# Performance work log

Measured on AMD Instinct MI355X. Metric: run time of the kernel, lower is better.

The kernel has to match this reference:

```python
import jax, jax.numpy as jnp
import numpy as np

WINDOW_SIZES = (1, 2, 3)
ALPHA = 0.2          # LeakyReLU negative slope
NEG = -9e15          # mask fill value from the torch code


def _xavier(key, shape, gain=np.sqrt(2.0)):
    fan_in, fan_out = shape[0], shape[1]
    std = gain * np.sqrt(2.0 / (fan_in + fan_out))
    return jax.random.normal(key, shape, jnp.float32) * std


def setup_inputs() -> dict:
    key = jax.random.key(0)
    k1, k2, k3, k4, k5 = jax.random.split(key, 5)
    T, B, D, F = 512, 64, 256, 256  # turns, batch, input_dim, output_dim (must match)
    return {
        "local_semantic_vectors": jax.random.normal(k1, (T, B, D), jnp.float32),
        "input_turns": jax.random.randint(k2, (B,), 0, T),  # turns[bt] <= T-1
        "W": _xavier(k3, (D, F)),
        "a1": _xavier(k4, (F, 1)),
        "a2": _xavier(k5, (F, 1)),
    }


def _window_mean(x, w):
    # x: [B, T, D] -> sliding-window mean over axis 1 (window w), zero-padded at end.
    B, T, D = x.shape
    xp = jnp.pad(x, ((0, 0), (0, w - 1), (0, 0)))
    acc = xp[:, :T]
    for j in range(1, w):  # w <= 3, tiny unrolled loop
        acc = acc + xp[:, j:j + T]
    return acc / w


def reference(local_semantic_vectors, input_turns, W, a1, a2):
    # local_semantic_vectors: [T, B, D] -> [B, T, D]
    x = jnp.swapaxes(local_semantic_vectors, 0, 1)
    B, T, D = x.shape
    t_idx = jnp.arange(T)

    num = jnp.zeros((B, W.shape[1]), jnp.float32)
    vws = jnp.zeros((B,), jnp.float32)  # number of window sizes with cnt > 0

    for w in WINDOW_SIZES:
        # number of valid windows per sample: t runs while w+t-1 <= turns
        cnt = jnp.maximum(input_turns - w + 2, 0)                  # [B]
        valid = t_idx[None, :] < cnt[:, None]                      # [B, T]

        # pooled window vectors, zero beyond cnt (max_turn padded to T;
        # padded rows are fully masked and dropped, so the result matches)
        pooled = jnp.where(valid[:, :, None], _window_mean(x, w), 0.0)  # [B, T, D]

        # GAT-style masked self-attention
        h = pooled @ W                                             # [B, T, F]
        f1 = h @ a1                                                # [B, T, 1]
        f2 = h @ a2                                                # [B, T, 1]
        e = jax.nn.leaky_relu(f1 + jnp.swapaxes(f2, 1, 2), ALPHA)  # [B, T, T]
        mask = valid[:, :, None] & valid[:, None, :]
        attn = jax.nn.softmax(jnp.where(mask, e, NEG), axis=-1)
        h_prime = attn @ h                                         # [B, T, F]

        # mean over the first cnt rows
        denom = jnp.maximum(cnt, 1).astype(jnp.float32)
        inter = (h_prime * valid[:, :, None]).sum(axis=1) / denom[:, None]  # [B, F]

        has = (cnt > 0).astype(jnp.float32)
        num = num + inter * has[:, None]
        vws = vws + has

    # cnt is non-increasing in w, so windows with cnt>0 are exactly the first vws;
    # vws >= 1 always (w=1 gives cnt = turns + 2 >= 2).
    return num / vws[:, None]
```

## Files before the change

kernel.cpp:

```cpp
#include <hip/hip_runtime.h>
#include <math.h>

#define T_DIM 512
#define B_DIM 64
#define D_DIM 256
#define F_DIM 256
#define ALPHA 0.2f
#define L2E 1.44269504089f
#define NEGL -1.0e38f

#define U_OFF 0
#define V_OFF 256
#define P_OFF 512
#define Q_OFF (P_OFF + B_DIM * T_DIM)
#define FC_OFF (Q_OFF + B_DIM * T_DIM)

__device__ __forceinline__ float dot4(float4 a, float4 b) {
    return a.x * b.x + a.y * b.y + a.z * b.z + a.w * b.w;
}

__device__ __forceinline__ float dpp_sum(float x) {
    union { float f; int i; } a, t;
    a.f = x;
    t.i = __builtin_amdgcn_update_dpp(0, a.i, 0x111, 0xf, 0xf, true); a.f += t.f;
    t.i = __builtin_amdgcn_update_dpp(0, a.i, 0x112, 0xf, 0xf, true); a.f += t.f;
    t.i = __builtin_amdgcn_update_dpp(0, a.i, 0x114, 0xf, 0xf, true); a.f += t.f;
    t.i = __builtin_amdgcn_update_dpp(0, a.i, 0x118, 0xf, 0xf, true); a.f += t.f;
    t.i = __builtin_amdgcn_update_dpp(0, a.i, 0x142, 0xf, 0xf, true); a.f += t.f;
    t.i = __builtin_amdgcn_update_dpp(0, a.i, 0x143, 0xf, 0xf, true); a.f += t.f;
    return a.f;
}

__global__ __launch_bounds__(256) void g_uv(const float* __restrict__ W,
                                            const float* __restrict__ a1,
                                            const float* __restrict__ a2,
                                            float* __restrict__ ws,
                                            float* __restrict__ out) {
    int tid = threadIdx.x;
    out[blockIdx.x * 256 + tid] = 0.f;
    int wave = tid >> 6, lane = tid & 63;
    int d = blockIdx.x * 4 + wave;
    float4 wv = ((const float4*)(W + (size_t)d * F_DIM))[lane];
    float4 a1v = ((const float4*)a1)[lane];
    float4 a2v = ((const float4*)a2)[lane];
    float p = dpp_sum(dot4(wv, a1v));
    float q = dpp_sum(dot4(wv, a2v));
    if (lane == 63) {
        ws[U_OFF + d] = p;
        ws[V_OFF + d] = q;
    }
}

__global__ __launch_bounds__(512) void g_pq(const float* __restrict__ x,
                                            const int* __restrict__ turns,
                                            float* __restrict__ ws) {
    __shared__ float su[D_DIM], sv[D_DIM];
    int tid = threadIdx.x;
    if (tid < 64) ((float4*)su)[tid] = ((const float4*)(ws + U_OFF))[tid];
    else if (tid < 128) ((float4*)sv)[tid - 64] = ((const float4*)(ws + V_OFF))[tid - 64];
    __syncthreads();
    int lane = tid & 63;
    int gw = blockIdx.x * 8 + (tid >> 6);
    int b = gw & 63;
    int tbase = gw >> 6;
    int tn = turns[b];
    float4 uv = ((const float4*)su)[lane];
    float4 vv = ((const float4*)sv)[lane];
    float4 xv[8];
#pragma unroll
    for (int k = 0; k < 8; ++k) {
        int t = min(tbase + k * 64, tn);
        xv[k] = ((const float4*)x)[((size_t)t * B_DIM + b) * (D_DIM / 4) + lane];
    }
#pragma unroll
    for (int k = 0; k < 8; ++k) {
        int t = tbase + k * 64;
        if (t <= tn) {
            float pp = dpp_sum(dot4(xv[k], uv));
            float qq = dpp_sum(dot4(xv[k], vv));
            if (lane == 63) {
                ws[P_OFF + b * T_DIM + t] = pp;
                ws[Q_OFF + b * T_DIM + t] = qq;
            }
        }
    }
}

__global__ __launch_bounds__(1024) void g_row(const int* __restrict__ turns,
                                              float* __restrict__ ws) {
    int bi = blockIdx.x, tid = threadIdx.x;
    int b = bi / 12, rem = bi % 12;
    int w = (rem >> 2) + 1, ic = rem & 3;
    int tn = turns[b];
    int cnt = tn - w + 2;
    if (cnt > T_DIM) cnt = T_DIM;
    float2* FC = (float2*)(ws + FC_OFF) + ((w - 1) * B_DIM + b) * T_DIM;
    if (cnt <= 0) return;
    __shared__ float sp[T_DIM], sq[T_DIM], f2L[T_DIM];
    __shared__ float part[8][128];
    __shared__ float redm[8];
    if (tid < 128) ((float4*)sp)[tid] = ((const float4*)(ws + P_OFF + b * T_DIM))[tid];
    else if (tid < 256) ((float4*)sq)[tid - 128] = ((const float4*)(ws + Q_OFF + b * T_DIM))[tid - 128];
    __syncthreads();
    float scale = L2E / (float)w;
    int wave = tid >> 6, lane = tid & 63;
    if (tid < 512) {
        int j = tid;
        float v = NEGL;
        if (j < cnt) {
            float a = sq[j];
            if (w > 1) a += sq[j + 1];
            if (w > 2) a += sq[j + 2];
            v = a * scale;
        }
        f2L[j] = v;
        float m = v;
        for (int off = 32; off > 0; off >>= 1) m = fmaxf(m, __shfl_down(m, off));
        if (lane == 0) redm[wave] = m;
    }
    __syncthreads();
    float M = redm[0];
#pragma unroll
    for (int k = 1; k < 8; ++k) M = fmaxf(M, redm[k]);

    int il = tid & 127, oct = tid >> 7;
    int i = ic * 128 + il;
    float r = 0.f;
    if (i < cnt) {
        float a = sp[i];
        if (w > 1) a += sp[i + 1];
        if (w > 2) a += sp[i + 2];
        float f1 = a * scale;
        float s0 = f1 + M;
        float mrow = fmaxf(s0, ALPHA * s0);
        const float4* fv = (const float4*)(f2L + oct * 64);
#pragma unroll 4
        for (int k = 0; k < 16; ++k) {
            float4 f = fv[k];
            float sa = f1 + f.x, sb = f1 + f.y, sc = f1 + f.z, sd = f1 + f.w;
            sa = fmaxf(sa, ALPHA * sa); sb = fmaxf(sb, ALPHA * sb);
            sc = fmaxf(sc, ALPHA * sc); sd = fmaxf(sd, ALPHA * sd);
            r += __builtin_amdgcn_exp2f(sa - mrow) + __builtin_amdgcn_exp2f(sb - mrow)
               + __builtin_amdgcn_exp2f(sc - mrow) + __builtin_amdgcn_exp2f(sd - mrow);
        }
    }
    part[oct][il] = r;
    __syncthreads();
    if (tid < 128) {
        int i2 = ic * 128 + tid;
        float2 pr = make_float2(0.f, 3.0e38f);
        if (i2 < cnt) {
            float rt = part[0][tid];
#pragma unroll
            for (int k = 1; k < 8; ++k) rt += part[k][tid];
            float a = sp[i2];
            if (w > 1) a += sp[i2 + 1];
            if (w > 2) a += sp[i2 + 2];
            float f1 = a * scale;
            float s0 = f1 + M;
            float mrow = fmaxf(s0, ALPHA * s0);
            pr = make_float2(f1, mrow + __builtin_amdgcn_logf(rt));
        }
        FC[i2] = pr;
    }
}

__global__ __launch_bounds__(512) void g_colzout(const float* __restrict__ x,
                                                 const int* __restrict__ turns,
                                                 const float* __restrict__ W,
                                                 const float* __restrict__ ws,
                                                 float* __restrict__ out) {
    int b = blockIdx.x >> 2, chunk = blockIdx.x & 3;
    int tn = turns[b];
    int t0 = chunk * 128;
    if (t0 > tn) return;
    int tid = threadIdx.x;
    __shared__ float sq[T_DIM];
    __shared__ float4 fcs4[3][T_DIM / 2];
    __shared__ float Gs[3][132];
    __shared__ float partq[128][4];
    __shared__ float part2[2][128];
    __shared__ float Cs[128];
    __shared__ float4 zp[512];
    __shared__ float Zs[D_DIM];
    __shared__ float ored[512];

    if (tid < 128) ((float4*)sq)[tid] = ((const float4*)(ws + Q_OFF + b * T_DIM))[tid];
    for (int k = tid; k < 3 * 256; k += 512) {
        int wi = k >> 8, kk = k & 255;
        fcs4[wi][kk] = ((const float4*)(ws + FC_OFF))[(wi * B_DIM + b) * 256 + kk];
    }
    __syncthreads();

    for (int w = 1; w <= 3; ++w) {
        int cw = tn - w + 2;
        if (cw > T_DIM) cw = T_DIM;
        bool act = cw > 0;
        float scale = L2E / (float)w;
        if (act) {
            {
                int jj = tid >> 2, iq = tid & 3;
                int j = t0 + jj;
                float acc = 0.f;
                if (j < cw) {
                    float a = sq[j];
                    if (w > 1) a += sq[j + 1];
                    if (w > 2) a += sq[j + 2];
                    float f2j = a * scale;
                    const float4* fv = fcs4[w - 1] + iq * 64;
                    for (int k = 0; k < 64; ++k) {
                        float4 f = fv[k];
                        float sa = f.x + f2j, sb = f.z + f2j;
                        sa = fmaxf(sa, ALPHA * sa); sb = fmaxf(sb, ALPHA * sb);
                        acc += __builtin_amdgcn_exp2f(sa - f.y)
                             + __builtin_amdgcn_exp2f(sb - f.w);
                    }
                }
                partq[jj][iq] = acc;
            }
            if (tid < 256) {
                int e = tid >> 7, q2 = tid & 127;
                int j2 = t0 - 2 + e;
                float acc = 0.f;
                if (j2 >= 0 && j2 < cw) {
                    float a = sq[j2];
                    if (w > 1) a += sq[j2 + 1];
                    if (w > 2) a += sq[j2 + 2];
                    float f2j = a * scale;
                    const float4* fv = fcs4[w - 1] + q2 * 2;
#pragma unroll
                    for (int k = 0; k < 2; ++k) {
                        float4 f = fv[k];
                        float sa = f.x + f2j, sb = f.z + f2j;
                        sa = fmaxf(sa, ALPHA * sa); sb = fmaxf(sb, ALPHA * sb);
                        acc += __builtin_amdgcn_exp2f(sa - f.y)
                             + __builtin_amdgcn_exp2f(sb - f.w);
                    }
                }
                part2[e][q2] = acc;
            }
        }
        __syncthreads();
        if (act) {
            float invc = 1.0f / (float)cw;
            if (tid < 128) {
                int j = t0 + tid;
                float s = partq[tid][0] + partq[tid][1] + partq[tid][2] + partq[tid][3];
                Gs[w - 1][2 + tid] = (j < cw) ? s * invc : 0.f;
            } else if (tid < 130) {
                int e = tid - 128;
                int j2 = t0 - 2 + e;
                float s = 0.f;
                for (int k = 0; k < 128; ++k) s += part2[e][k];
                Gs[w - 1][e] = (j2 >= 0 && j2 < cw) ? s * invc : 0.f;
            }
        } else if (tid < 132) {
            Gs[w - 1][tid] = 0.f;
        }
        __syncthreads();
    }

    if (tid < 128) {
        float g1 = Gs[0][2 + tid];
        float g2 = Gs[1][2 + tid] + Gs[1][1 + tid];
        float g3 = Gs[2][2 + tid] + Gs[2][1 + tid] + Gs[2][tid];
        float vws = 1.f + (tn >= 1 ? 1.f : 0.f) + (tn >= 2 ? 1.f : 0.f);
        Cs[tid] = (g1 + 0.5f * g2 + (1.0f / 3.0f) * g3) / vws;
    }
    __syncthreads();

    int wave = tid >> 6, lane = tid & 63;
    float4 z = make_float4(0.f, 0.f, 0.f, 0.f);
    {
        size_t base = ((size_t)(t0 + wave * 16) * B_DIM + b) * (D_DIM / 4) + lane;
#pragma unroll 8
        for (int tt = 0; tt < 16; ++tt) {
            float c = Cs[wave * 16 + tt];
            float4 xv = ((const float4*)x)[base + (size_t)tt * (B_DIM * D_DIM / 4)];
            z.x += c * xv.x; z.y += c * xv.y; z.z += c * xv.z; z.w += c * xv.w;
        }
    }
    zp[tid] = z;
    __syncthreads();
    if (tid < 64) {
        float4 a = zp[tid];
#pragma unroll
        for (int k = 1; k < 8; ++k) {
            float4 bb = zp[k * 64 + tid];
            a.x += bb.x; a.y += bb.y; a.z += bb.z; a.w += bb.w;
        }
        ((float4*)Zs)[tid] = a;
    }
    __syncthreads();
    int f = tid & 255, dh = tid >> 8;
    float acc = 0.f;
#pragma unroll 8
    for (int dd = dh * 128; dd < dh * 128 + 128; ++dd)
        acc += Zs[dd] * W[(size_t)dd * F_DIM + f];
    ored[tid] = acc;
    __syncthreads();
    if (tid < 256)
        atomicAdd(&out[b * F_DIM + tid], ored[tid] + ored[tid + 256]);
}

extern "C" void kernel_launch(void* const* d_in, const int* in_sizes, int n_in,
                              void* d_out, int out_size, void* d_ws, size_t ws_size,
                              hipStream_t stream) {
    const float* x = (const float*)d_in[0];
    const int* turns = (const int*)d_in[1];
    const float* W = (const float*)d_in[2];
    const float* a1 = (const float*)d_in[3];
    const float* a2 = (const float*)d_in[4];
    float* out = (float*)d_out;
    float* ws = (float*)d_ws;

    g_uv<<<B_DIM, 256, 0, stream>>>(W, a1, a2, ws, out);
    g_pq<<<512, 512, 0, stream>>>(x, turns, ws);
    g_row<<<B_DIM * 12, 1024, 0, stream>>>(turns, ws);
    g_colzout<<<B_DIM * 4, 512, 0, stream>>>(x, turns, W, ws, out);
}
```

Measured before the change: 47.00 us.

## Fuse uv, pq and row-softmax kernels into one per-batch front kernel

Merges three kernels (W·a projection, per-turn p/q dot products, row log-sum-exp) into a single kernel with one 1024-thread block per batch element. Intermediates p, q, u and v stay in shared memory rather than round-tripping through global workspace, and two launches are removed. In exchange, every block recomputes W·a1/W·a2 redundantly and parallelism drops from hundreds of blocks to 64, each doing serial work over all three window sizes.

Result: slower. 74.52 us (+58.5%).

```diff
diff --git a/kernel.cpp b/kernel.cpp
--- a/kernel.cpp
+++ b/kernel.cpp
@@ -9,10 +9,7 @@
 #define L2E 1.44269504089f
 #define NEGL -1.0e38f
 
-#define U_OFF 0
-#define V_OFF 256
-#define P_OFF 512
-#define Q_OFF (P_OFF + B_DIM * T_DIM)
+#define Q_OFF 0
 #define FC_OFF (Q_OFF + B_DIM * T_DIM)
 
 __device__ __forceinline__ float dot4(float4 a, float4 b) {
@@ -31,137 +28,138 @@
     return a.f;
 }
 
-__global__ __launch_bounds__(256) void g_uv(const float* __restrict__ W,
-                                            const float* __restrict__ a1,
-                                            const float* __restrict__ a2,
-                                            float* __restrict__ ws,
-                                            float* __restrict__ out) {
-    int tid = threadIdx.x;
-    out[blockIdx.x * 256 + tid] = 0.f;
+__global__ __launch_bounds__(1024) void g_front(const float* __restrict__ x,
+                                                const int* __restrict__ turns,
+                                                const float* __restrict__ W,
+                                                const float* __restrict__ a1,
+                                                const float* __restrict__ a2,
+                                                float* __restrict__ ws,
+                                                float* __restrict__ out) {
+    int b = blockIdx.x, tid = threadIdx.x;
     int wave = tid >> 6, lane = tid & 63;
-    int d = blockIdx.x * 4 + wave;
-    float4 wv = ((const float4*)(W + (size_t)d * F_DIM))[lane];
-    float4 a1v = ((const float4*)a1)[lane];
-    float4 a2v = ((const float4*)a2)[lane];
-    float p = dpp_sum(dot4(wv, a1v));
-    float q = dpp_sum(dot4(wv, a2v));
-    if (lane == 63) {
-        ws[U_OFF + d] = p;
-        ws[V_OFF + d] = q;
-    }
-}
-
-__global__ __launch_bounds__(512) void g_pq(const float* __restrict__ x,
-                                            const int* __restrict__ turns,
-                                            float* __restrict__ ws) {
-    __shared__ float su[D_DIM], sv[D_DIM];
-    int tid = threadIdx.x;
-    if (tid < 64) ((float4*)su)[tid] = ((const float4*)(ws + U_OFF))[tid];
-    else if (tid < 128) ((float4*)sv)[tid - 64] = ((const float4*)(ws + V_OFF))[tid - 64];
-    __syncthreads();
-    int lane = tid & 63;
-    int gw = blockIdx.x * 8 + (tid >> 6);
-    int b = gw & 63;
-    int tbase = gw >> 6;
+    __shared__ float a1s[F_DIM], a2s[F_DIM], su[D_DIM], sv[D_DIM];
+    __shared__ float sp[T_DIM], sq[T_DIM], f2L[T_DIM];
+    __shared__ float part[2][T_DIM];
+    __shared__ float redm[8];
+
+    if (tid < 256) out[b * F_DIM + tid] = 0.f;
+    if (tid < 64) ((float4*)a1s)[tid] = ((const float4*)a1)[tid];
+    else if (tid < 128) ((float4*)a2s)[tid - 64] = ((const float4*)a2)[tid - 64];
+    __syncthreads();
+
+    {
+        float4 A = ((const float4*)a1s)[lane];
+        float4 Bv = ((const float4*)a2s)[lane];
+        float4 wv[8];
+#pragma unroll
+        for (int c = 0; c < 2; ++c) {
+#pragma unroll
+            for (int k = 0; k < 8; ++k) {
+                int d = wave + 16 * (c * 8 + k);
+                wv[k] = ((const float4*)(W + (size_t)d * F_DIM))[lane];
+            }
+#pragma unroll
+            for (int k = 0; k < 8; ++k) {
+                int d = wave + 16 * (c * 8 + k);
+                float p = dpp_sum(dot4(wv[k], A));
+                float q = dpp_sum(dot4(wv[k], Bv));
+                if (lane == 63) { su[d] = p; sv[d] = q; }
+            }
+        }
+    }
+    __syncthreads();
+
     int tn = turns[b];
-    float4 uv = ((const float4*)su)[lane];
-    float4 vv = ((const float4*)sv)[lane];
-    float4 xv[8];
-#pragma unroll
-    for (int k = 0; k < 8; ++k) {
-        int t = min(tbase + k * 64, tn);
-        xv[k] = ((const float4*)x)[((size_t)t * B_DIM + b) * (D_DIM / 4) + lane];
-    }
-#pragma unroll
-    for (int k = 0; k < 8; ++k) {
-        int t = tbase + k * 64;
-        if (t <= tn) {
-            float pp = dpp_sum(dot4(xv[k], uv));
-            float qq = dpp_sum(dot4(xv[k], vv));
-            if (lane == 63) {
-                ws[P_OFF + b * T_DIM + t] = pp;
-                ws[Q_OFF + b * T_DIM + t] = qq;
-            }
-        }
-    }
-}
-
-__global__ __launch_bounds__(1024) void g_row(const int* __restrict__ turns,
-                                              float* __restrict__ ws) {
-    int bi = blockIdx.x, tid = threadIdx.x;
-    int b = bi / 12, rem = bi % 12;
-    int w = (rem >> 2) + 1, ic = rem & 3;
-    int tn = turns[b];
-    int cnt = tn - w + 2;
-    if (cnt > T_DIM) cnt = T_DIM;
-    float2* FC = (float2*)(ws + FC_OFF) + ((w - 1) * B_DIM + b) * T_DIM;
-    if (cnt <= 0) return;
-    __shared__ float sp[T_DIM], sq[T_DIM], f2L[T_DIM];
-    __shared__ float part[8][128];
-    __shared__ float redm[8];
-    if (tid < 128) ((float4*)sp)[tid] = ((const float4*)(ws + P_OFF + b * T_DIM))[tid];
-    else if (tid < 256) ((float4*)sq)[tid - 128] = ((const float4*)(ws + Q_OFF + b * T_DIM))[tid - 128];
-    __syncthreads();
-    float scale = L2E / (float)w;
-    int wave = tid >> 6, lane = tid & 63;
-    if (tid < 512) {
-        int j = tid;
-        float v = NEGL;
-        if (j < cnt) {
-            float a = sq[j];
-            if (w > 1) a += sq[j + 1];
-            if (w > 2) a += sq[j + 2];
-            v = a * scale;
-        }
-        f2L[j] = v;
-        float m = v;
-        for (int off = 32; off > 0; off >>= 1) m = fmaxf(m, __shfl_down(m, off));
-        if (lane == 0) redm[wave] = m;
-    }
-    __syncthreads();
-    float M = redm[0];
-#pragma unroll
-    for (int k = 1; k < 8; ++k) M = fmaxf(M, redm[k]);
-
-    int il = tid & 127, oct = tid >> 7;
-    int i = ic * 128 + il;
-    float r = 0.f;
-    if (i < cnt) {
-        float a = sp[i];
-        if (w > 1) a += sp[i + 1];
-        if (w > 2) a += sp[i + 2];
-        float f1 = a * scale;
-        float s0 = f1 + M;
-        float mrow = fmaxf(s0, ALPHA * s0);
-        const float4* fv = (const float4*)(f2L + oct * 64);
+    {
+        float4 uu = ((const float4*)su)[lane];
+        float4 vv = ((const float4*)sv)[lane];
+        float4 xv[8];
+#pragma unroll
+        for (int c = 0; c < 4; ++c) {
+#pragma unroll
+            for (int k = 0; k < 8; ++k) {
+                int t = min(wave + 16 * (c * 8 + k), tn);
+                xv[k] = ((const float4*)x)[((size_t)t * B_DIM + b) * (D_DIM / 4) + lane];
+            }
+#pragma unroll
+            for (int k = 0; k < 8; ++k) {
+                int t = wave + 16 * (c * 8 + k);
+                if (t <= tn) {
+                    float pp = dpp_sum(dot4(xv[k], uu));
+                    float qq = dpp_sum(dot4(xv[k], vv));
+                    if (lane == 63) {
+                        sp[t] = pp; sq[t] = qq;
+                        ws[Q_OFF + b * T_DIM + t] = qq;
+                    }
+                }
+            }
+        }
+    }
+    __syncthreads();
+
+    for (int w = 1; w <= 3; ++w) {
+        int cnt = tn - w + 2;
+        if (cnt > T_DIM) cnt = T_DIM;
+        if (cnt <= 0) continue;
+        float scale = L2E / (float)w;
+        if (tid < 512) {
+            int j = tid;
+            float v = NEGL;
+            if (j < cnt) {
+                float a = sq[j];
+                if (w > 1) a += sq[j + 1];
+                if (w > 2) a += sq[j + 2];
+                v = a * scale;
+            }
+            f2L[j] = v;
+            float m = v;
+            for (int off = 32; off > 0; off >>= 1) m = fmaxf(m, __shfl_down(m, off));
+            if (lane == 0) redm[wave] = m;
+        }
+        __syncthreads();
+        float M = redm[0];
+#pragma unroll
+        for (int k = 1; k < 8; ++k) M = fmaxf(M, redm[k]);
+
+        {
+            int i = tid & 511, jh = tid >> 9;
+            float r = 0.f;
+            if (i < cnt) {
+                float a = sp[i];
+                if (w > 1) a += sp[i + 1];
+                if (w > 2) a += sp[i + 2];
+                float f1 = a * scale;
+                float s0 = f1 + M;
+                float mrow = fmaxf(s0, ALPHA * s0);
+                const float4* fv = (const float4*)(f2L + jh * 256);
 #pragma unroll 4
-        for (int k = 0; k < 16; ++k) {
-            float4 f = fv[k];
-            float sa = f1 + f.x, sb = f1 + f.y, sc = f1 + f.z, sd = f1 + f.w;
-            sa = fmaxf(sa, ALPHA * sa); sb = fmaxf(sb, ALPHA * sb);
-            sc = fmaxf(sc, ALPHA * sc); sd = fmaxf(sd, ALPHA * sd);
-            r += __builtin_amdgcn_exp2f(sa - mrow) + __builtin_amdgcn_exp2f(sb - mrow)
-               + __builtin_amdgcn_exp2f(sc - mrow) + __builtin_amdgcn_exp2f(sd - mrow);
-        }
-    }
-    part[oct][il] = r;
-    __syncthreads();
-    if (tid < 128) {
-        int i2 = ic * 128 + tid;
-        float2 pr = make_float2(0.f, 3.0e38f);
-        if (i2 < cnt) {
-            float rt = part[0][tid];
-#pragma unroll
-            for (int k = 1; k < 8; ++k) rt += part[k][tid];
-            float a = sp[i2];
-            if (w > 1) a += sp[i2 + 1];
-            if (w > 2) a += sp[i2 + 2];
-            float f1 = a * scale;
-            float s0 = f1 + M;
-            float mrow = fmaxf(s0, ALPHA * s0);
-            pr = make_float2(f1, mrow + __builtin_amdgcn_logf(rt));
-        }
-        FC[i2] = pr;
+                for (int k = 0; k < 64; ++k) {
+                    float4 f = fv[k];
+                    float sa = f1 + f.x, sb = f1 + f.y, sc = f1 + f.z, sd = f1 + f.w;
+                    sa = fmaxf(sa, ALPHA * sa); sb = fmaxf(sb, ALPHA * sb);
+                    sc = fmaxf(sc, ALPHA * sc); sd = fmaxf(sd, ALPHA * sd);
+                    r += __builtin_amdgcn_exp2f(sa - mrow) + __builtin_amdgcn_exp2f(sb - mrow)
+                       + __builtin_amdgcn_exp2f(sc - mrow) + __builtin_amdgcn_exp2f(sd - mrow);
+                }
+            }
+            part[jh][i] = r;
+        }
+        __syncthreads();
+        if (tid < 512) {
+            int i = tid;
+            float2 pr = make_float2(0.f, 3.0e38f);
+            if (i < cnt) {
+                float a = sp[i];
+                if (w > 1) a += sp[i + 1];
+                if (w > 2) a += sp[i + 2];
+                float f1 = a * scale;
+                float s0 = f1 + M;
+                float mrow = fmaxf(s0, ALPHA * s0);
+                pr = make_float2(f1, mrow + __builtin_amdgcn_logf(part[0][i] + part[1][i]));
+            }
+            ((float2*)(ws + FC_OFF))[((w - 1) * B_DIM + b) * T_DIM + i] = pr;
+        }
+        __syncthreads();
     }
 }
 
@@ -314,8 +312,6 @@
     float* out = (float*)d_out;
     float* ws = (float*)d_ws;
 
-    g_uv<<<B_DIM, 256, 0, stream>>>(W, a1, a2, ws, out);
-    g_pq<<<512, 512, 0, stream>>>(x, turns, ws);
-    g_row<<<B_DIM * 12, 1024, 0, stream>>>(turns, ws);
+    g_front<<<B_DIM, 1024, 0, stream>>>(x, turns, W, a1, a2, ws, out);
     g_colzout<<<B_DIM * 4, 512, 0, stream>>>(x, turns, W, ws, out);
 }
```

## Fuse p/q projection into row-softmax kernel, looping window sizes per block

Applied to the files above, without the earlier changes.

Merges the g_pq and g_row kernels into one g_rowpq kernel with 256 blocks, one per (batch, 128-row chunk). Each block recomputes q over all turns of its batch and p over its own row range (plus a halo) directly into shared memory, then loops over the three window sizes. This drops a kernel launch and the global round-trip of p. The cost is redundant reads of x and q dot products, since each batch's full q is recomputed by four blocks, and there are fewer blocks running serial work per window.

After: 56.40 us. +20.0%, slower.

```diff
diff --git a/kernel.cpp b/kernel.cpp
--- a/kernel.cpp
+++ b/kernel.cpp
@@ -11,8 +11,7 @@
 
 #define U_OFF 0
 #define V_OFF 256
-#define P_OFF 512
-#define Q_OFF (P_OFF + B_DIM * T_DIM)
+#define Q_OFF 512
 #define FC_OFF (Q_OFF + B_DIM * T_DIM)
 
 __device__ __forceinline__ float dot4(float4 a, float4 b) {
@@ -51,117 +50,129 @@
     }
 }
 
-__global__ __launch_bounds__(512) void g_pq(const float* __restrict__ x,
-                                            const int* __restrict__ turns,
-                                            float* __restrict__ ws) {
+__global__ __launch_bounds__(1024) void g_rowpq(const float* __restrict__ x,
+                                                const int* __restrict__ turns,
+                                                float* __restrict__ ws) {
+    int b = blockIdx.x >> 2, ic = blockIdx.x & 3;
+    int tid = threadIdx.x, wave = tid >> 6, lane = tid & 63;
+    int i0 = ic * 128;
     __shared__ float su[D_DIM], sv[D_DIM];
-    int tid = threadIdx.x;
-    if (tid < 64) ((float4*)su)[tid] = ((const float4*)(ws + U_OFF))[tid];
-    else if (tid < 128) ((float4*)sv)[tid - 64] = ((const float4*)(ws + V_OFF))[tid - 64];
-    __syncthreads();
-    int lane = tid & 63;
-    int gw = blockIdx.x * 8 + (tid >> 6);
-    int b = gw & 63;
-    int tbase = gw >> 6;
-    int tn = turns[b];
-    float4 uv = ((const float4*)su)[lane];
-    float4 vv = ((const float4*)sv)[lane];
-    float4 xv[8];
-#pragma unroll
-    for (int k = 0; k < 8; ++k) {
-        int t = min(tbase + k * 64, tn);
-        xv[k] = ((const float4*)x)[((size_t)t * B_DIM + b) * (D_DIM / 4) + lane];
-    }
-#pragma unroll
-    for (int k = 0; k < 8; ++k) {
-        int t = tbase + k * 64;
-        if (t <= tn) {
-            float pp = dpp_sum(dot4(xv[k], uv));
-            float qq = dpp_sum(dot4(xv[k], vv));
-            if (lane == 63) {
-                ws[P_OFF + b * T_DIM + t] = pp;
-                ws[Q_OFF + b * T_DIM + t] = qq;
-            }
-        }
-    }
-}
-
-__global__ __launch_bounds__(1024) void g_row(const int* __restrict__ turns,
-                                              float* __restrict__ ws) {
-    int bi = blockIdx.x, tid = threadIdx.x;
-    int b = bi / 12, rem = bi % 12;
-    int w = (rem >> 2) + 1, ic = rem & 3;
-    int tn = turns[b];
-    int cnt = tn - w + 2;
-    if (cnt > T_DIM) cnt = T_DIM;
-    float2* FC = (float2*)(ws + FC_OFF) + ((w - 1) * B_DIM + b) * T_DIM;
-    if (cnt <= 0) return;
     __shared__ float sp[T_DIM], sq[T_DIM], f2L[T_DIM];
     __shared__ float part[8][128];
     __shared__ float redm[8];
-    if (tid < 128) ((float4*)sp)[tid] = ((const float4*)(ws + P_OFF + b * T_DIM))[tid];
-    else if (tid < 256) ((float4*)sq)[tid - 128] = ((const float4*)(ws + Q_OFF + b * T_DIM))[tid - 128];
-    __syncthreads();
-    float scale = L2E / (float)w;
-    int wave = tid >> 6, lane = tid & 63;
-    if (tid < 512) {
-        int j = tid;
-        float v = NEGL;
-        if (j < cnt) {
-            float a = sq[j];
-            if (w > 1) a += sq[j + 1];
-            if (w > 2) a += sq[j + 2];
-            v = a * scale;
-        }
-        f2L[j] = v;
-        float m = v;
-        for (int off = 32; off > 0; off >>= 1) m = fmaxf(m, __shfl_down(m, off));
-        if (lane == 0) redm[wave] = m;
-    }
-    __syncthreads();
-    float M = redm[0];
-#pragma unroll
-    for (int k = 1; k < 8; ++k) M = fmaxf(M, redm[k]);
-
-    int il = tid & 127, oct = tid >> 7;
-    int i = ic * 128 + il;
-    float r = 0.f;
-    if (i < cnt) {
-        float a = sp[i];
-        if (w > 1) a += sp[i + 1];
-        if (w > 2) a += sp[i + 2];
-        float f1 = a * scale;
-        float s0 = f1 + M;
-        float mrow = fmaxf(s0, ALPHA * s0);
-        const float4* fv = (const float4*)(f2L + oct * 64);
-#pragma unroll 4
-        for (int k = 0; k < 16; ++k) {
-            float4 f = fv[k];
-            float sa = f1 + f.x, sb = f1 + f.y, sc = f1 + f.z, sd = f1 + f.w;
-            sa = fmaxf(sa, ALPHA * sa); sb = fmaxf(sb, ALPHA * sb);
-            sc = fmaxf(sc, ALPHA * sc); sd = fmaxf(sd, ALPHA * sd);
-            r += __builtin_amdgcn_exp2f(sa - mrow) + __builtin_amdgcn_exp2f(sb - mrow)
-               + __builtin_amdgcn_exp2f(sc - mrow) + __builtin_amdgcn_exp2f(sd - mrow);
-        }
-    }
-    part[oct][il] = r;
-    __syncthreads();
-    if (tid < 128) {
-        int i2 = ic * 128 + tid;
-        float2 pr = make_float2(0.f, 3.0e38f);
-        if (i2 < cnt) {
-            float rt = part[0][tid];
-#pragma unroll
-            for (int k = 1; k < 8; ++k) rt += part[k][tid];
-            float a = sp[i2];
-            if (w > 1) a += sp[i2 + 1];
-            if (w > 2) a += sp[i2 + 2];
+    if (tid < 64) ((float4*)su)[tid] = ((const float4*)(ws + U_OFF))[tid];
+    else if (tid < 128) ((float4*)sv)[tid - 64] = ((const float4*)(ws + V_OFF))[tid - 64];
+    __syncthreads();
+    int tn = turns[b];
+    float4 uu = ((const float4*)su)[lane];
+    float4 vv = ((const float4*)sv)[lane];
+
+    {
+        float4 xv[8];
+#pragma unroll
+        for (int c = 0; c < 4; ++c) {
+#pragma unroll
+            for (int k = 0; k < 8; ++k) {
+                int t = min(wave + 16 * (c * 8 + k), tn);
+                xv[k] = ((const float4*)x)[((size_t)t * B_DIM + b) * (D_DIM / 4) + lane];
+            }
+#pragma unroll
+            for (int k = 0; k < 8; ++k) {
+                int t = wave + 16 * (c * 8 + k);
+                if (t <= tn) {
+                    float qq = dpp_sum(dot4(xv[k], vv));
+                    if (lane == 63) {
+                        sq[t] = qq;
+                        if (t >= i0 && t < i0 + 128)
+                            ws[Q_OFF + b * T_DIM + t] = qq;
+                    }
+                }
+            }
+        }
+    }
+    {
+        float4 xv[9];
+#pragma unroll
+        for (int k = 0; k < 9; ++k) {
+            int t = min(min(i0 + wave + 16 * k, tn), T_DIM - 1);
+            xv[k] = ((const float4*)x)[((size_t)t * B_DIM + b) * (D_DIM / 4) + lane];
+        }
+#pragma unroll
+        for (int k = 0; k < 9; ++k) {
+            int t = i0 + wave + 16 * k;
+            if (t < T_DIM && t <= tn) {
+                float pp = dpp_sum(dot4(xv[k], uu));
+                if (lane == 63) sp[t] = pp;
+            }
+        }
+    }
+    __syncthreads();
+
+    for (int w = 1; w <= 3; ++w) {
+        int cnt = tn - w + 2;
+        if (cnt > T_DIM) cnt = T_DIM;
+        if (cnt <= 0) continue;
+        float scale = L2E / (float)w;
+        if (tid < 512) {
+            int j = tid;
+            float v = NEGL;
+            if (j < cnt) {
+                float a = sq[j];
+                if (w > 1) a += sq[j + 1];
+                if (w > 2) a += sq[j + 2];
+                v = a * scale;
+            }
+            f2L[j] = v;
+            float m = v;
+            for (int off = 32; off > 0; off >>= 1) m = fmaxf(m, __shfl_down(m, off));
+            if (lane == 0) redm[wave] = m;
+        }
+        __syncthreads();
+        float M = redm[0];
+#pragma unroll
+        for (int k = 1; k < 8; ++k) M = fmaxf(M, redm[k]);
+
+        int il = tid & 127, oct = tid >> 7;
+        int i = i0 + il;
+        float r = 0.f;
+        if (i < cnt) {
+            float a = sp[i];
+            if (w > 1) a += sp[i + 1];
+            if (w > 2) a += sp[i + 2];
             float f1 = a * scale;
             float s0 = f1 + M;
             float mrow = fmaxf(s0, ALPHA * s0);
-            pr = make_float2(f1, mrow + __builtin_amdgcn_logf(rt));
-        }
-        FC[i2] = pr;
+            const float4* fv = (const float4*)(f2L + oct * 64);
+#pragma unroll 4
+            for (int k = 0; k < 16; ++k) {
+                float4 f = fv[k];
+                float sa = f1 + f.x, sb = f1 + f.y, sc = f1 + f.z, sd = f1 + f.w;
+                sa = fmaxf(sa, ALPHA * sa); sb = fmaxf(sb, ALPHA * sb);
+                sc = fmaxf(sc, ALPHA * sc); sd = fmaxf(sd, ALPHA * sd);
+                r += __builtin_amdgcn_exp2f(sa - mrow) + __builtin_amdgcn_exp2f(sb - mrow)
+                   + __builtin_amdgcn_exp2f(sc - mrow) + __builtin_amdgcn_exp2f(sd - mrow);
+            }
+        }
+        part[oct][il] = r;
+        __syncthreads();
+        if (tid < 128) {
+            int i2 = i0 + tid;
+            float2 pr = make_float2(0.f, 3.0e38f);
+            if (i2 < cnt) {
+                float rt = part[0][tid];
+#pragma unroll
+                for (int k = 1; k < 8; ++k) rt += part[k][tid];
+                float a = sp[i2];
+                if (w > 1) a += sp[i2 + 1];
+                if (w > 2) a += sp[i2 + 2];
+                float f1 = a * scale;
+                float s0 = f1 + M;
+                float mrow = fmaxf(s0, ALPHA * s0);
+                pr = make_float2(f1, mrow + __builtin_amdgcn_logf(rt));
+            }
+            ((float2*)(ws + FC_OFF))[((w - 1) * B_DIM + b) * T_DIM + i2] = pr;
+        }
+        __syncthreads();
     }
 }
 
@@ -315,7 +326,6 @@
     float* ws = (float*)d_ws;
 
     g_uv<<<B_DIM, 256, 0, stream>>>(W, a1, a2, ws, out);
-    g_pq<<<512, 512, 0, stream>>>(x, turns, ws);
-    g_row<<<B_DIM * 12, 1024, 0, stream>>>(turns, ws);
+    g_rowpq<<<256, 1024, 0, stream>>>(x, turns, ws);
     g_colzout<<<B_DIM * 4, 512, 0, stream>>>(x, turns, W, ws, out);
 }
```
